# Kernel tuning notes

Hardware: AMD Instinct MI355X
Metric: run time of the kernel (lower is better)

## Reference

```python
import jax, jax.numpy as jnp
import numpy as np

EPS = 1e-6

def _rmsnorm(x, w):
    # fp32 RMSNorm over last dim
    var = jnp.mean(x * x, axis=-1, keepdims=True)
    return w * (x * jax.lax.rsqrt(var + EPS))

def setup_inputs() -> dict:
    key = jax.random.key(0)
    ks = jax.random.split(key, 6)
    S, D, H = 4096, 1024, 16
    HD = D // H
    return {
        "hidden_states": jax.random.normal(ks[0], (S, D), jnp.float32),
        "qkv_w": jax.random.normal(ks[1], (3 * D, D), jnp.float32) * 0.02,
        "qkv_b": jnp.zeros((3 * D,), jnp.float32),
        "proj_w": jax.random.normal(ks[2], (D, D), jnp.float32) * 0.02,
        "proj_b": jnp.zeros((D,), jnp.float32),
        "q_norm_w": jnp.ones((D,), jnp.float32),
        "k_norm_w": jnp.ones((D,), jnp.float32),
        "rotary_freqs": jax.random.normal(ks[3], (S, HD // 2), jnp.float32),
        "cu_seqlens": jnp.array([0, 1024, 2048, 3072, 4096], jnp.int32),
        "num_heads": 16,
    }

def reference(hidden_states, qkv_w, qkv_b, proj_w, proj_b, q_norm_w, k_norm_w, rotary_freqs, cu_seqlens, num_heads):
    S, D = hidden_states.shape
    H = num_heads
    hd = D // H
    # QKV projection
    qkv = hidden_states @ qkv_w.T + qkv_b           # [S, 3D]
    qkv = qkv.reshape(S, 3, H, hd)
    q, k, v = qkv[:, 0], qkv[:, 1], qkv[:, 2]       # each [S, H, hd]
    # QK RMSNorm over the flattened hidden dim (InternVL style)
    q = _rmsnorm(q.reshape(S, D), q_norm_w).reshape(S, H, hd)
    k = _rmsnorm(k.reshape(S, D), k_norm_w).reshape(S, H, hd)
    # RoPE: freqs [S, hd/2] -> cos/sin [S, 1, hd] (tiled, not interleaved)
    cos = jnp.cos(rotary_freqs)
    sin = jnp.sin(rotary_freqs)
    cos = jnp.concatenate([cos, cos], axis=-1)[:, None, :]
    sin = jnp.concatenate([sin, sin], axis=-1)[:, None, :]
    def rope(t):
        x1, x2 = jnp.split(t, 2, axis=-1)
        rot = jnp.concatenate([-x2, x1], axis=-1)
        return t * cos + rot * sin
    q = rope(q)
    k = rope(k)
    # Block-diagonal mask from cu_seqlens: same-segment tokens attend
    seg = jnp.searchsorted(cu_seqlens[1:], jnp.arange(S), side='right')  # [S]
    mask = seg[:, None] == seg[None, :]                                   # [S, S]
    scale = 1.0 / jnp.sqrt(jnp.float32(hd))
    scores = jnp.einsum('shd,thd->hst', q, k) * scale                     # [H, S, S]
    scores = jnp.where(mask[None], scores, jnp.float32(-1e30))
    probs = jax.nn.softmax(scores, axis=-1)
    out = jnp.einsum('hst,thd->shd', probs, v).reshape(S, D)
    return out @ proj_w.T + proj_b
```

## Files before the change

kernel.cpp:

```cpp
#include <hip/hip_runtime.h>
#include <hip/hip_bf16.h>

#define S 4096
#define D 1024
#define NH 16
#define HD 64

typedef float f32x4 __attribute__((ext_vector_type(4)));
typedef float f32x16 __attribute__((ext_vector_type(16)));
typedef __bf16 bf16x8 __attribute__((ext_vector_type(8)));

#define MFMA16(a, b, c) __builtin_amdgcn_mfma_f32_16x16x32_bf16((a), (b), (c), 0, 0, 0)
#define MFMA32(a, b, c) __builtin_amdgcn_mfma_f32_32x32x16_bf16((a), (b), (c), 0, 0, 0)

__device__ __forceinline__ unsigned short f2bf(float f) {
  unsigned int u = __builtin_bit_cast(unsigned int, f);
  u += 0x7FFFu + ((u >> 16) & 1u);
  return (unsigned short)(u >> 16);
}

__device__ __forceinline__ float bf2f(unsigned short u) {
  unsigned int x = ((unsigned int)u) << 16;
  return __builtin_bit_cast(float, x);
}

__device__ __forceinline__ unsigned cvtpk(float lo, float hi) {
  unsigned r;
  asm("v_cvt_pk_bf16_f32 %0, %1, %2" : "=v"(r) : "v"(lo), "v"(hi));
  return r;
}

__device__ __forceinline__ void pl32swap(unsigned& a, unsigned& b) {
#if __has_builtin(__builtin_amdgcn_permlane32_swap)
  typedef unsigned u32x2 __attribute__((ext_vector_type(2)));
  u32x2 r = __builtin_amdgcn_permlane32_swap(a, b, false, false);
  a = r.x;
  b = r.y;
#else
  asm volatile("v_permlane32_swap_b32 %0, %1" : "+v"(a), "+v"(b));
#endif
}

typedef __attribute__((address_space(1))) void GAS;
typedef __attribute__((address_space(3))) void LAS;

__device__ __forceinline__ void gld_lds16(const unsigned short* g, unsigned short* l) {
  __builtin_amdgcn_global_load_lds((GAS*)g, (LAS*)l, 16, 0, 0);
}

__global__ void cvt3(const float* __restrict__ a, unsigned short* __restrict__ ao,
                     const float* __restrict__ b, unsigned short* __restrict__ bo,
                     const float* __restrict__ c, unsigned short* __restrict__ co) {
  int i = blockIdx.x * blockDim.x + threadIdx.x;
  const float* in;
  unsigned short* out;
  int j;
  if (i < 1048576) { in = a; out = ao; j = i; }
  else if (i < 1835008) { in = b; out = bo; j = i - 1048576; }
  else { in = c; out = co; j = i - 1835008; }
  float4 v = ((const float4*)in)[j];
  ushort4 u;
  u.x = f2bf(v.x); u.y = f2bf(v.y); u.z = f2bf(v.z); u.w = f2bf(v.w);
  ((ushort4*)out)[j] = u;
}

__device__ __forceinline__ int xcd_swz(int bid, int nwg) {
  int q = nwg >> 3;
  return (bid & 7) * q + (bid >> 3);
}

#define DSTEP_S(RA, RB, SA, SB, KN, VM)                                          \
  {                                                                              \
    bf16x8 af[4], bfv[4];                                                        \
    _Pragma("unroll") for (int mf = 0; mf < 4; ++mf)                             \
        af[mf] = *(const bf16x8*)&RA[(wr * 64 + mf * 16 + l15) * 32 + l4 * 8];   \
    _Pragma("unroll") for (int nf = 0; nf < 4; ++nf)                             \
        bfv[nf] = *(const bf16x8*)&RB[(wc * 64 + nf * 16 + l15) * 32 + l4 * 8];  \
    gld_lds16(Ab + (size_t)r0 * 1024 + (KN) + o0, &SA[w * 512]);                 \
    gld_lds16(Ab + (size_t)r1 * 1024 + (KN) + o1, &SA[2048 + w * 512]);          \
    gld_lds16(Bb + (size_t)r0 * 1024 + (KN) + o0, &SB[w * 512]);                 \
    gld_lds16(Bb + (size_t)r1 * 1024 + (KN) + o1, &SB[2048 + w * 512]);          \
    __builtin_amdgcn_s_setprio(1);                                               \
    _Pragma("unroll") for (int mf = 0; mf < 4; ++mf)                             \
        _Pragma("unroll") for (int nf = 0; nf < 4; ++nf)                         \
            acc[mf][nf] = MFMA16(af[mf], bfv[nf], acc[mf][nf]);                  \
    __builtin_amdgcn_s_setprio(0);                                               \
    asm volatile("s_waitcnt vmcnt(" VM ")" ::: "memory");                        \
    __builtin_amdgcn_s_barrier();                                                \
  }

#define DSTEP_N(RA, RB, VM)                                                      \
  {                                                                              \
    bf16x8 af[4], bfv[4];                                                        \
    _Pragma("unroll") for (int mf = 0; mf < 4; ++mf)                             \
        af[mf] = *(const bf16x8*)&RA[(wr * 64 + mf * 16 + l15) * 32 + l4 * 8];   \
    _Pragma("unroll") for (int nf = 0; nf < 4; ++nf)                             \
        bfv[nf] = *(const bf16x8*)&RB[(wc * 64 + nf * 16 + l15) * 32 + l4 * 8];  \
    __builtin_amdgcn_s_setprio(1);                                               \
    _Pragma("unroll") for (int mf = 0; mf < 4; ++mf)                             \
        _Pragma("unroll") for (int nf = 0; nf < 4; ++nf)                         \
            acc[mf][nf] = MFMA16(af[mf], bfv[nf], acc[mf][nf]);                  \
    __builtin_amdgcn_s_setprio(0);                                               \
    asm volatile("s_waitcnt vmcnt(" VM ")" ::: "memory");                        \
    __builtin_amdgcn_s_barrier();                                                \
  }

#define DSTEP_LAST(RA, RB)                                                       \
  {                                                                              \
    bf16x8 af[4], bfv[4];                                                        \
    _Pragma("unroll") for (int mf = 0; mf < 4; ++mf)                             \
        af[mf] = *(const bf16x8*)&RA[(wr * 64 + mf * 16 + l15) * 32 + l4 * 8];   \
    _Pragma("unroll") for (int nf = 0; nf < 4; ++nf)                             \
        bfv[nf] = *(const bf16x8*)&RB[(wc * 64 + nf * 16 + l15) * 32 + l4 * 8];  \
    __builtin_amdgcn_s_setprio(1);                                               \
    _Pragma("unroll") for (int mf = 0; mf < 4; ++mf)                             \
        _Pragma("unroll") for (int nf = 0; nf < 4; ++nf)                         \
            acc[mf][nf] = MFMA16(af[mf], bfv[nf], acc[mf][nf]);                  \
    __builtin_amdgcn_s_setprio(0);                                               \
  }

#define GEMM_PRO_LOOP()                                                          \
  gld_lds16(Ab + (size_t)r0 * 1024 + o0, &As0[w * 512]);                         \
  gld_lds16(Ab + (size_t)r1 * 1024 + o1, &As0[2048 + w * 512]);                  \
  gld_lds16(Bb + (size_t)r0 * 1024 + o0, &Bs0[w * 512]);                         \
  gld_lds16(Bb + (size_t)r1 * 1024 + o1, &Bs0[2048 + w * 512]);                  \
  gld_lds16(Ab + (size_t)r0 * 1024 + 32 + o0, &As1[w * 512]);                    \
  gld_lds16(Ab + (size_t)r1 * 1024 + 32 + o1, &As1[2048 + w * 512]);             \
  gld_lds16(Bb + (size_t)r0 * 1024 + 32 + o0, &Bs1[w * 512]);                    \
  gld_lds16(Bb + (size_t)r1 * 1024 + 32 + o1, &Bs1[2048 + w * 512]);             \
  asm volatile("s_waitcnt vmcnt(4)" ::: "memory");                               \
  __builtin_amdgcn_s_barrier();                                                  \
  _Pragma("unroll 1") for (int k0 = 0; k0 < 960; k0 += 96) {                     \
    DSTEP_S(As0, Bs0, As2, Bs2, k0 + 64, "4")                                    \
    DSTEP_S(As1, Bs1, As0, Bs0, k0 + 96, "4")                                    \
    DSTEP_S(As2, Bs2, As1, Bs1, k0 + 128, "4")                                   \
  }                                                                              \
  DSTEP_N(As0, Bs0, "0")                                                         \
  DSTEP_LAST(As1, Bs1)

__global__ __launch_bounds__(256, 3) void gemm_qkv(const unsigned short* __restrict__ A,
                                                   const unsigned short* __restrict__ B,
                                                   const float* __restrict__ bias,
                                                   unsigned short* __restrict__ qk,
                                                   unsigned short* __restrict__ vt) {
  __shared__ __align__(16) unsigned short As0[4096], As1[4096], As2[4096];
  __shared__ __align__(16) unsigned short Bs0[4096], Bs1[4096], Bs2[4096];
  __shared__ __align__(16) unsigned short tr[128 * 17];
  const int t = threadIdx.x;
  const int lane = t & 63;
  const int w = t >> 6;
  const int wr = w >> 1, wc = w & 1;
  const int l15 = lane & 15, l4 = lane >> 4;
  const int bid = blockIdx.y * 24 + blockIdx.x;
  const int r8 = bid & 7, i = bid >> 3;
  const int by = (r8 >> 1) * 8 + i / 12;
  const int bx = (r8 & 1) * 12 + i % 12;
  const int m0 = by * 128, n0 = bx * 128;

  f32x4 acc[4][4] = {};

  const int r0 = t >> 2, o0 = (t & 3) * 8;
  const int r1 = (256 + t) >> 2, o1 = ((256 + t) & 3) * 8;
  const unsigned short* Ab = A + (size_t)m0 * 1024;
  const unsigned short* Bb = B + (size_t)n0 * 1024;

  GEMM_PRO_LOOP()

  if (n0 < 2048) {
#pragma unroll
    for (int mf = 0; mf < 4; ++mf)
#pragma unroll
      for (int nf = 0; nf < 4; ++nf) {
        int rr = m0 + wr * 64 + mf * 16 + l4 * 4;
        int cc = n0 + wc * 64 + nf * 16 + l15;
        float bv = bias[cc];
#pragma unroll
        for (int j = 0; j < 4; ++j)
          qk[(size_t)(rr + j) * 2048 + cc] = f2bf(acc[mf][nf][j] + bv);
      }
  } else {
    const int h0 = (n0 - 2048) >> 6;
#pragma unroll
    for (int ch = 0; ch < 8; ++ch) {
      __syncthreads();
      if (wc == (ch >> 2)) {
        const int nf = ch & 3;
        const float bv = bias[n0 + (ch >> 2) * 64 + nf * 16 + l15];
#pragma unroll
        for (int mf = 0; mf < 4; ++mf) {
          int srow = wr * 64 + mf * 16 + l4 * 4;
#pragma unroll
          for (int j = 0; j < 4; ++j)
            tr[(srow + j) * 17 + l15] = f2bf(acc[mf][nf][j] + bv);
        }
      }
      __syncthreads();
      const int hh = h0 + (ch >> 2);
      const int dbase = (ch & 3) * 16;
#pragma unroll
      for (int i2 = 0; i2 < 2; ++i2) {
        int g = i2 * 256 + t;
        int dp = g >> 5, sg = g & 31;
        ushort4 u;
        u.x = tr[(sg * 4 + 0) * 17 + dp];
        u.y = tr[(sg * 4 + 1) * 17 + dp];
        u.z = tr[(sg * 4 + 2) * 17 + dp];
        u.w = tr[(sg * 4 + 3) * 17 + dp];
        *(ushort4*)(vt + (size_t)hh * HD * S + (size_t)(dbase + dp) * S + m0 + sg * 4) = u;
      }
    }
  }
}

__global__ __launch_bounds__(256, 3) void gemm_bt(const unsigned short* __restrict__ A,
                                                  const unsigned short* __restrict__ B,
                                                  const float* __restrict__ bias,
                                                  float* __restrict__ C,
                                                  int M, int N, int K, int gx) {
  __shared__ __align__(16) unsigned short As0[4096], As1[4096], As2[4096];
  __shared__ __align__(16) unsigned short Bs0[4096], Bs1[4096], Bs2[4096];
  const int t = threadIdx.x;
  const int lane = t & 63;
  const int w = t >> 6;
  const int wr = w >> 1, wc = w & 1;
  const int l15 = lane & 15, l4 = lane >> 4;
  const int nwg = gridDim.x * gridDim.y;
  const int nbid = xcd_swz(blockIdx.y * gx + blockIdx.x, nwg);
  const int m0 = (nbid / gx) * 128, n0 = (nbid % gx) * 128;

  f32x4 acc[4][4] = {};

  const int r0 = t >> 2, o0 = (t & 3) * 8;
  const int r1 = (256 + t) >> 2, o1 = ((256 + t) & 3) * 8;
  const unsigned short* Ab = A + (size_t)m0 * 1024;
  const unsigned short* Bb = B + (size_t)n0 * 1024;

  GEMM_PRO_LOOP()

#pragma unroll
  for (int mf = 0; mf < 4; ++mf) {
#pragma unroll
    for (int nf = 0; nf < 4; ++nf) {
      int rr = m0 + wr * 64 + mf * 16 + l4 * 4;
      int cc = n0 + wc * 64 + nf * 16 + l15;
      float bv = bias[cc];
#pragma unroll
      for (int j = 0; j < 4; ++j)
        C[(size_t)(rr + j) * N + cc] = acc[mf][nf][j] + bv;
    }
  }
}

__global__ __launch_bounds__(256) void norm_rope(const unsigned short* __restrict__ qk,
                                                 const float* __restrict__ qw,
                                                 const float* __restrict__ kw,
                                                 const float* __restrict__ fr,
                                                 unsigned short* __restrict__ qo,
                                                 unsigned short* __restrict__ ko) {
  __shared__ float buf[1024];
  __shared__ float red[4];
  const int s = blockIdx.x, t = threadIdx.x;
  const int lane = t & 63, w = t >> 6;
  const int e = t * 4;
  const int hh = e >> 6, dd = e & 63;
  const float* frow = fr + (size_t)s * 32;
  float cs[4], sn[4];
#pragma unroll
  for (int i = 0; i < 4; ++i) {
    float f = frow[(dd + i) & 31];
    cs[i] = cosf(f);
    sn[i] = sinf(f);
  }
  for (int part = 0; part < 2; ++part) {
    const unsigned short* row = qk + (size_t)s * 2048 + part * 1024;
    const float* wvp = part ? kw : qw;
    unsigned short* op = part ? ko : qo;
    const float oscale = part ? 1.0f : 0.18033688011112042f;
    ushort4 uv = *(const ushort4*)(row + e);
    float vx = bf2f(uv.x), vy = bf2f(uv.y), vz = bf2f(uv.z), vw = bf2f(uv.w);
    float ssq = vx * vx + vy * vy + vz * vz + vw * vw;
#pragma unroll
    for (int off = 1; off < 64; off <<= 1) ssq += __shfl_xor(ssq, off, 64);
    if (part) __syncthreads();
    if (lane == 0) red[w] = ssq;
    __syncthreads();
    float inv = rsqrtf((red[0] + red[1] + red[2] + red[3]) * (1.0f / 1024.0f) + 1e-6f);
    float4 wv = *(const float4*)(wvp + e);
    buf[e + 0] = vx * inv * wv.x;
    buf[e + 1] = vy * inv * wv.y;
    buf[e + 2] = vz * inv * wv.z;
    buf[e + 3] = vw * inv * wv.w;
    __syncthreads();
    unsigned short ov[4];
#pragma unroll
    for (int i = 0; i < 4; ++i) {
      int di = dd + i;
      float x = buf[e + i];
      float rot = (di < 32) ? -buf[e + i + 32] : buf[e + i - 32];
      ov[i] = f2bf((x * cs[i] + rot * sn[i]) * oscale);
    }
    unsigned short* dst = op + (size_t)hh * S * HD + (size_t)s * HD + dd;
    dst[0] = ov[0]; dst[1] = ov[1]; dst[2] = ov[2]; dst[3] = ov[3];
  }
}

__device__ __forceinline__ void qk_tile32(f32x16& s0, f32x16& s1,
                                          const unsigned short* Kbuf,
                                          const bf16x8* qB, int l31, int l5) {
  const int x7 = l31 & 7;
#pragma unroll
  for (int c = 0; c < 4; ++c) {
    const int ch = (2 * c + l5) ^ x7;
    bf16x8 ka0 = *(const bf16x8*)&Kbuf[l31 * 64 + ch * 8];
    bf16x8 ka1 = *(const bf16x8*)&Kbuf[(32 + l31) * 64 + ch * 8];
    s0 = MFMA32(ka0, qB[c], s0);
    s1 = MFMA32(ka1, qB[c], s1);
  }
}

__global__ __launch_bounds__(256) void attn_kernel(const unsigned short* __restrict__ q,
                                                   const unsigned short* __restrict__ k,
                                                   const unsigned short* __restrict__ vt,
                                                   unsigned short* __restrict__ aout) {
  __shared__ __align__(16) unsigned short Ks[2][4096];
  __shared__ __align__(16) unsigned short Vs[3][4096];
  const int bid = blockIdx.x;
  const int xcd = bid & 7;
  const int idx = bid >> 3;
  const int gw = idx >> 3, qt = idx & 7;
  const int g = xcd * 8 + gw;
  const int h = g >> 2, seg = g & 3;
  const int t = threadIdx.x, lane = t & 63, w = t >> 6;
  const int l31 = lane & 31, l5 = lane >> 5;
  const size_t hb = (size_t)h * S * HD;
  const int q0 = seg * 1024 + qt * 128 + w * 32;
  const int kvbase = seg * 1024;

  const int sr = t >> 3;
  const int scb = (t & 7) ^ (sr & 7);
  const unsigned short* ksrcA = k + hb + (size_t)(kvbase + sr) * HD + scb * 8;
  const unsigned short* ksrcB = ksrcA + 32 * HD;
  const unsigned short* vsrcA = vt + (size_t)h * HD * S + (size_t)sr * S + kvbase + scb * 8;
  const unsigned short* vsrcB = vsrcA + (size_t)32 * S;

  const unsigned short* qp = q + hb + (size_t)(q0 + l31) * HD + l5 * 8;
  bf16x8 qB[4];
#pragma unroll
  for (int c = 0; c < 4; ++c) qB[c] = *(const bf16x8*)(qp + 16 * c);

  f32x16 o0 = {}, o1 = {};
  float m = -1e30f, l = 0.f;

  gld_lds16(ksrcA, &Ks[0][w * 512]);
  gld_lds16(ksrcB, &Ks[0][2048 + w * 512]);
  gld_lds16(ksrcA + 4096, &Ks[1][w * 512]);
  gld_lds16(ksrcB + 4096, &Ks[1][2048 + w * 512]);
  gld_lds16(vsrcA, &Vs[0][w * 512]);
  gld_lds16(vsrcB, &Vs[0][2048 + w * 512]);
  gld_lds16(vsrcA + 64, &Vs[1][w * 512]);
  gld_lds16(vsrcB + 64, &Vs[1][2048 + w * 512]);
  __syncthreads();

  f32x16 cur0 = {}, cur1 = {};
  qk_tile32(cur0, cur1, Ks[0], qB, l31, l5);
  __syncthreads();

#pragma unroll
  for (int it = 0; it < 16; ++it) {
    if (it < 14) {
      gld_lds16(ksrcA + (it + 2) * 4096, &Ks[it & 1][w * 512]);
      gld_lds16(ksrcB + (it + 2) * 4096, &Ks[it & 1][2048 + w * 512]);
      gld_lds16(vsrcA + (it + 2) * 64, &Vs[(it + 2) % 3][w * 512]);
      gld_lds16(vsrcB + (it + 2) * 64, &Vs[(it + 2) % 3][2048 + w * 512]);
    }
    f32x16 nxt0 = {}, nxt1 = {};
    if (it < 15) {
      __builtin_amdgcn_s_setprio(1);
      qk_tile32(nxt0, nxt1, Ks[(it + 1) & 1], qB, l31, l5);
      __builtin_amdgcn_s_setprio(0);
      __builtin_amdgcn_sched_barrier(0);
    }
    float mm[16];
#pragma unroll
    for (int i = 0; i < 16; ++i) mm[i] = fmaxf(cur0[i], cur1[i]);
#pragma unroll
    for (int st = 8; st > 0; st >>= 1)
#pragma unroll
      for (int i = 0; i < 8; ++i)
        if (i < st) mm[i] = fmaxf(mm[i], mm[i + st]);
    float lmax = fmaxf(mm[0], __shfl_xor(mm[0], 32, 64));
    if (!__all(lmax <= m + 8.0f)) {
      const float mn = fmaxf(m, lmax);
      const float corr = exp2f(m - mn);
      m = mn;
      l *= corr;
#pragma unroll
      for (int i = 0; i < 16; ++i) { o0[i] *= corr; o1[i] *= corr; }
    }
    unsigned pk0[8], pk1[8];
    float ls0 = 0.f, ls1 = 0.f;
#pragma unroll
    for (int i = 0; i < 8; ++i) {
      float a0 = exp2f(cur0[2 * i] - m), a1 = exp2f(cur0[2 * i + 1] - m);
      float b0 = exp2f(cur1[2 * i] - m), b1 = exp2f(cur1[2 * i + 1] - m);
      ls0 += a0 + a1;
      ls1 += b0 + b1;
      pk0[i] = cvtpk(a0, a1);
      pk1[i] = cvtpk(b0, b1);
    }
    l += ls0 + ls1;
    bf16x8 pB[4];
#pragma unroll
    for (int c = 0; c < 4; ++c) {
      const int cl = c & 1;
      unsigned w0, w1, w2, w3;
      if (c < 2) { w0 = pk0[4 * cl + 0]; w1 = pk0[4 * cl + 1]; w2 = pk0[4 * cl + 2]; w3 = pk0[4 * cl + 3]; }
      else       { w0 = pk1[4 * cl + 0]; w1 = pk1[4 * cl + 1]; w2 = pk1[4 * cl + 2]; w3 = pk1[4 * cl + 3]; }
      pl32swap(w0, w2);
      pl32swap(w1, w3);
      uint4 bw;
      bw.x = w0; bw.y = w1; bw.z = w2; bw.w = w3;
      pB[c] = __builtin_bit_cast(bf16x8, bw);
    }
    const unsigned short* Vbuf = Vs[it % 3];
    const int x7 = l31 & 7;
    __builtin_amdgcn_s_setprio(1);
#pragma unroll
    for (int c = 0; c < 4; ++c) {
      const int ch = (2 * c + l5) ^ x7;
      bf16x8 va0 = *(const bf16x8*)&Vbuf[l31 * 64 + ch * 8];
      bf16x8 va1 = *(const bf16x8*)&Vbuf[(32 + l31) * 64 + ch * 8];
      o0 = MFMA32(va0, pB[c], o0);
      o1 = MFMA32(va1, pB[c], o1);
    }
    __builtin_amdgcn_s_setprio(0);
    __syncthreads();
    cur0 = nxt0;
    cur1 = nxt1;
  }

  l += __shfl_xor(l, 32, 64);
  const float invl = 1.0f / l;
#pragma unroll
  for (int blk = 0; blk < 2; ++blk) {
#pragma unroll
    for (int rg = 0; rg < 4; ++rg) {
      const f32x16& o = blk ? o1 : o0;
      ushort4 u;
      u.x = f2bf(o[4 * rg + 0] * invl);
      u.y = f2bf(o[4 * rg + 1] * invl);
      u.z = f2bf(o[4 * rg + 2] * invl);
      u.w = f2bf(o[4 * rg + 3] * invl);
      const int dcol = 32 * blk + 8 * rg + 4 * l5;
      *(ushort4*)(aout + (size_t)(q0 + l31) * D + h * 64 + dcol) = u;
    }
  }
}

extern "C" void kernel_launch(void* const* d_in, const int* in_sizes, int n_in,
                              void* d_out, int out_size, void* d_ws, size_t ws_size,
                              hipStream_t stream) {
  const float* hidden = (const float*)d_in[0];
  const float* qkvw   = (const float*)d_in[1];
  const float* qkvb   = (const float*)d_in[2];
  const float* projw  = (const float*)d_in[3];
  const float* projb  = (const float*)d_in[4];
  const float* qnw    = (const float*)d_in[5];
  const float* knw    = (const float*)d_in[6];
  const float* freqs  = (const float*)d_in[7];
  float* out = (float*)d_out;
  char* ws = (char*)d_ws;

  unsigned short* hb  = (unsigned short*)(ws + 0);
  unsigned short* wb  = (unsigned short*)(ws + (8u << 20));
  unsigned short* pb  = (unsigned short*)(ws + (14u << 20));
  unsigned short* qk  = (unsigned short*)(ws + (16u << 20));
  unsigned short* vtb = (unsigned short*)(ws + (32u << 20));
  unsigned short* qb  = (unsigned short*)(ws + (40u << 20));
  unsigned short* kb  = (unsigned short*)(ws + (48u << 20));
  unsigned short* ab  = (unsigned short*)(ws + (56u << 20));

  cvt3<<<8192, 256, 0, stream>>>(hidden, hb, qkvw, wb, projw, pb);
  gemm_qkv<<<dim3(24, 32), 256, 0, stream>>>(hb, wb, qkvb, qk, vtb);
  norm_rope<<<4096, 256, 0, stream>>>(qk, qnw, knw, freqs, qb, kb);
  attn_kernel<<<512, 256, 0, stream>>>(qb, kb, vtb, ab);
  gemm_bt<<<dim3(8, 32), 256, 0, stream>>>(ab, pb, projb, out, 4096, 1024, 1024, 8);
}
```

Measured before the change: 117.9 us.

## Split attention KV range in two halves and merge with combine kernel

The attention kernel now splits each segment's 1024 keys into two 512-key halves, doubling the grid to 1024 blocks. Each half writes unnormalized fp32 partial outputs plus row max and sum, and a new combine kernel merges them with the log-sum-exp rescaling and emits bf16. This is meant to raise occupancy and parallelism on the many-CU GPU, at the cost of extra fp32 global traffic and another launch. Separately, norm_rope computes cos/sin once per row into shared memory instead of once per thread.

```diff
diff --git a/kernel.cpp b/kernel.cpp
--- a/kernel.cpp
+++ b/kernel.cpp
@@ -259,17 +259,24 @@
                                                  unsigned short* __restrict__ ko) {
   __shared__ float buf[1024];
   __shared__ float red[4];
+  __shared__ float scs[32], ssn[32];
   const int s = blockIdx.x, t = threadIdx.x;
   const int lane = t & 63, w = t >> 6;
   const int e = t * 4;
   const int hh = e >> 6, dd = e & 63;
   const float* frow = fr + (size_t)s * 32;
+  if (t < 32) {
+    float f = frow[t];
+    scs[t] = cosf(f);
+    ssn[t] = sinf(f);
+  }
+  __syncthreads();
   float cs[4], sn[4];
 #pragma unroll
   for (int i = 0; i < 4; ++i) {
-    float f = frow[(dd + i) & 31];
-    cs[i] = cosf(f);
-    sn[i] = sinf(f);
+    int fi = (dd + i) & 31;
+    cs[i] = scs[fi];
+    sn[i] = ssn[fi];
   }
   for (int part = 0; part < 2; ++part) {
     const unsigned short* row = qk + (size_t)s * 2048 + part * 1024;
@@ -321,20 +328,24 @@
 __global__ __launch_bounds__(256) void attn_kernel(const unsigned short* __restrict__ q,
                                                    const unsigned short* __restrict__ k,
                                                    const unsigned short* __restrict__ vt,
-                                                   unsigned short* __restrict__ aout) {
+                                                   float* __restrict__ O1,
+                                                   float* __restrict__ O2,
+                                                   float2* __restrict__ lmb) {
   __shared__ __align__(16) unsigned short Ks[2][4096];
   __shared__ __align__(16) unsigned short Vs[3][4096];
   const int bid = blockIdx.x;
   const int xcd = bid & 7;
   const int idx = bid >> 3;
-  const int gw = idx >> 3, qt = idx & 7;
+  const int half = idx & 1;
+  const int qt = (idx >> 1) & 7;
+  const int gw = idx >> 4;
   const int g = xcd * 8 + gw;
   const int h = g >> 2, seg = g & 3;
   const int t = threadIdx.x, lane = t & 63, w = t >> 6;
   const int l31 = lane & 31, l5 = lane >> 5;
   const size_t hb = (size_t)h * S * HD;
   const int q0 = seg * 1024 + qt * 128 + w * 32;
-  const int kvbase = seg * 1024;
+  const int kvbase = seg * 1024 + half * 512;
 
   const int sr = t >> 3;
   const int scb = (t & 7) ^ (sr & 7);
@@ -366,15 +377,15 @@
   __syncthreads();
 
 #pragma unroll
-  for (int it = 0; it < 16; ++it) {
-    if (it < 14) {
+  for (int it = 0; it < 8; ++it) {
+    if (it < 6) {
       gld_lds16(ksrcA + (it + 2) * 4096, &Ks[it & 1][w * 512]);
       gld_lds16(ksrcB + (it + 2) * 4096, &Ks[it & 1][2048 + w * 512]);
       gld_lds16(vsrcA + (it + 2) * 64, &Vs[(it + 2) % 3][w * 512]);
       gld_lds16(vsrcB + (it + 2) * 64, &Vs[(it + 2) % 3][2048 + w * 512]);
     }
     f32x16 nxt0 = {}, nxt1 = {};
-    if (it < 15) {
+    if (it < 7) {
       __builtin_amdgcn_s_setprio(1);
       qk_tile32(nxt0, nxt1, Ks[(it + 1) & 1], qB, l31, l5);
       __builtin_amdgcn_s_setprio(0);
@@ -440,21 +451,49 @@
   }
 
   l += __shfl_xor(l, 32, 64);
-  const float invl = 1.0f / l;
+  float* Od = half ? O2 : O1;
 #pragma unroll
   for (int blk = 0; blk < 2; ++blk) {
 #pragma unroll
     for (int rg = 0; rg < 4; ++rg) {
       const f32x16& o = blk ? o1 : o0;
-      ushort4 u;
-      u.x = f2bf(o[4 * rg + 0] * invl);
-      u.y = f2bf(o[4 * rg + 1] * invl);
-      u.z = f2bf(o[4 * rg + 2] * invl);
-      u.w = f2bf(o[4 * rg + 3] * invl);
+      float4 u;
+      u.x = o[4 * rg + 0];
+      u.y = o[4 * rg + 1];
+      u.z = o[4 * rg + 2];
+      u.w = o[4 * rg + 3];
       const int dcol = 32 * blk + 8 * rg + 4 * l5;
-      *(ushort4*)(aout + (size_t)(q0 + l31) * D + h * 64 + dcol) = u;
-    }
-  }
+      *(float4*)(Od + (size_t)(q0 + l31) * D + h * 64 + dcol) = u;
+    }
+  }
+  if (lane < 32) {
+    float2 lm;
+    lm.x = l;
+    lm.y = m;
+    lmb[(size_t)(half * 16 + h) * S + q0 + l31] = lm;
+  }
+}
+
+__global__ __launch_bounds__(256) void attn_combine(const float* __restrict__ O1,
+                                                    const float* __restrict__ O2,
+                                                    const float2* __restrict__ lmb,
+                                                    unsigned short* __restrict__ ab) {
+  const int s = blockIdx.x, t = threadIdx.x;
+  const int col = t * 4;
+  const int h = col >> 6;
+  float2 A = lmb[(size_t)h * S + s];
+  float2 B = lmb[(size_t)(16 + h) * S + s];
+  float M = fmaxf(A.y, B.y);
+  float s1 = exp2f(A.y - M), s2 = exp2f(B.y - M);
+  float invl = 1.0f / (A.x * s1 + B.x * s2);
+  float4 a = *(const float4*)(O1 + (size_t)s * D + col);
+  float4 b = *(const float4*)(O2 + (size_t)s * D + col);
+  ushort4 u;
+  u.x = f2bf((a.x * s1 + b.x * s2) * invl);
+  u.y = f2bf((a.y * s1 + b.y * s2) * invl);
+  u.z = f2bf((a.z * s1 + b.z * s2) * invl);
+  u.w = f2bf((a.w * s1 + b.w * s2) * invl);
+  *(ushort4*)(ab + (size_t)s * D + col) = u;
 }
 
 extern "C" void kernel_launch(void* const* d_in, const int* in_sizes, int n_in,
@@ -479,10 +518,14 @@
   unsigned short* qb  = (unsigned short*)(ws + (40u << 20));
   unsigned short* kb  = (unsigned short*)(ws + (48u << 20));
   unsigned short* ab  = (unsigned short*)(ws + (56u << 20));
+  float*          Op1 = (float*)(ws + (16u << 20));
+  float*          Op2 = (float*)(ws + (64u << 20));
+  float2*         lmb = (float2*)(ws + (80u << 20));
 
   cvt3<<<8192, 256, 0, stream>>>(hidden, hb, qkvw, wb, projw, pb);
   gemm_qkv<<<dim3(24, 32), 256, 0, stream>>>(hb, wb, qkvb, qk, vtb);
   norm_rope<<<4096, 256, 0, stream>>>(qk, qnw, knw, freqs, qb, kb);
-  attn_kernel<<<512, 256, 0, stream>>>(qb, kb, vtb, ab);
+  attn_kernel<<<1024, 256, 0, stream>>>(qb, kb, vtb, Op1, Op2, lmb);
+  attn_combine<<<4096, 256, 0, stream>>>(Op1, Op2, lmb, ab);
   gemm_bt<<<dim3(8, 32), 256, 0, stream>>>(ab, pb, projb, out, 4096, 1024, 1024, 8);
 }
```

New measurement: 125.3 us. 6.2% more time.
